# Performance work log

Hardware: AMD Instinct MI355X
Metric: run time of the kernel (lower is better)

## Reference

```python
import jax, jax.numpy as jnp
import numpy as np

B, H, W, C = 8, 64, 64, 64
C8 = C // 8

def setup_inputs() -> dict:
    key = jax.random.key(0)
    ks = jax.random.split(key, 5)
    x = jax.random.normal(ks[0], (B, H, W, C), dtype=jnp.float32)
    # 1x1 conv kernels (fan-in scaled) + biases
    wq = jax.random.normal(ks[1], (C, C8), dtype=jnp.float32) / np.sqrt(C)
    wk = jax.random.normal(ks[2], (C, C8), dtype=jnp.float32) / np.sqrt(C)
    wv = jax.random.normal(ks[3], (C, C), dtype=jnp.float32) / np.sqrt(C)
    bq = jnp.zeros((C8,), dtype=jnp.float32)
    bk = jnp.zeros((C8,), dtype=jnp.float32)
    bv = jnp.zeros((C,), dtype=jnp.float32)
    gamma = jax.random.normal(ks[4], (), dtype=jnp.float32)
    return {"x": x, "wq": wq, "bq": bq, "wk": wk, "bk": bk,
            "wv": wv, "bv": bv, "gamma": gamma}

def reference(x, wq, bq, wk, bk, wv, bv, gamma):
    b, h, w, c = x.shape
    n = h * w
    # 1x1 convs == per-pixel linear projections
    q = (jnp.einsum('bhwc,cd->bhwd', x, wq) + bq).reshape(b, n, -1)  # [B,N,C/8]
    k = (jnp.einsum('bhwc,cd->bhwd', x, wk) + bk).reshape(b, n, -1)  # [B,N,C/8]
    v = (jnp.einsum('bhwc,cd->bhwd', x, wv) + bv).reshape(b, n, -1)  # [B,N,C]
    # Unscaled attention: softmax over keys (last axis), no 1/sqrt(d)
    attn = jax.nn.softmax(jnp.einsum('bnd,bmd->bnm', q, k), axis=-1)  # [B,N,N]
    out = jnp.einsum('bnm,bmc->bnc', attn, v).reshape(b, h, w, c)
    return out * gamma + x
```

## Files before the change

### kernel.cpp

```cpp
#include <hip/hip_runtime.h>
#include <hip/hip_bf16.h>


#define BB 8
#define NN 4096
#define CC 64
#define PSTRIDE 72
#define LOG2E 1.44269504088896f

typedef _Float16 f16;
typedef _Float16 half8 __attribute__((ext_vector_type(8)));
typedef _Float16 half4 __attribute__((ext_vector_type(4)));
typedef __fp16 fp16x2 __attribute__((ext_vector_type(2)));
typedef float floatx4 __attribute__((ext_vector_type(4)));

static __device__ inline half4 pack4(float a, float b, float c, float d) {
    fp16x2 lo = __builtin_amdgcn_cvt_pkrtz(a, b);
    fp16x2 hi = __builtin_amdgcn_cvt_pkrtz(c, d);
    unsigned int lou = __builtin_bit_cast(unsigned int, lo);
    unsigned int hiu = __builtin_bit_cast(unsigned int, hi);
    unsigned long long packed = (unsigned long long)lou | ((unsigned long long)hiu << 32);
    return __builtin_bit_cast(half4, packed);
}


__global__ __launch_bounds__(256) void proj_all_kernel(
    const float* __restrict__ x,
    const float* __restrict__ wq, const float* __restrict__ bq,
    const float* __restrict__ wk, const float* __restrict__ bk,
    const float* __restrict__ wv, const float* __restrict__ bv,
    f16* __restrict__ Qh, f16* __restrict__ Kf, f16* __restrict__ Vf,
    float* __restrict__ qn2, float* __restrict__ kn2)
{
    __shared__ alignas(16) f16 Ws[80][PSTRIDE];
    __shared__ float Bs[80];
    __shared__ alignas(16) f16 Vs[64][68];
    __shared__ alignas(16) f16 Ks[64][12];
    const int tid = threadIdx.x;

    for (int i = tid; i < 4096; i += 256) {
        int cin = i >> 6, cout = i & 63;
        Ws[cout][cin] = (f16)wv[i];
    }
    for (int i = tid; i < 512; i += 256) {
        int cin = i >> 3, c = i & 7;
        Ws[64 + c][cin] = (f16)(wq[i] * LOG2E);
        Ws[72 + c][cin] = (f16)wk[i];
    }
    if (tid < 80)
        Bs[tid] = (tid < 64) ? bv[tid]
                : (tid < 72 ? bq[tid - 64] * LOG2E : bk[tid - 72]);
    __syncthreads();

    const int wave = tid >> 6, lane = tid & 63;
    const int quad = lane >> 4, n16 = lane & 15;
    const long pb = (long)blockIdx.x * 64;
    const long p0 = pb + wave * 16;
    const int  b   = (int)(pb >> 12);
    const int  nnb = (int)(pb & 4095);

    half8 ax[2];
#pragma unroll
    for (int kh = 0; kh < 2; ++kh) {
        const float* xp = x + (p0 + n16) * 64 + kh * 32 + quad * 8;
        float4 x1 = *(const float4*)xp;
        float4 x2 = *(const float4*)(xp + 4);
        ax[kh][0] = (f16)x1.x; ax[kh][1] = (f16)x1.y;
        ax[kh][2] = (f16)x1.z; ax[kh][3] = (f16)x1.w;
        ax[kh][4] = (f16)x2.x; ax[kh][5] = (f16)x2.y;
        ax[kh][6] = (f16)x2.z; ax[kh][7] = (f16)x2.w;
    }

#pragma unroll
    for (int ct = 0; ct < 5; ++ct) {
        const int cout = (ct < 4) ? ct * 16 + n16 : 64 + n16;
        const float bias = Bs[cout];
        half8 b0 = *(const half8*)(&Ws[cout][quad * 8]);
        half8 b1 = *(const half8*)(&Ws[cout][32 + quad * 8]);
        floatx4 acc = {bias, bias, bias, bias};
        acc = __builtin_amdgcn_mfma_f32_16x16x32_f16(ax[0], b0, acc, 0, 0, 0);
        acc = __builtin_amdgcn_mfma_f32_16x16x32_f16(ax[1], b1, acc, 0, 0, 0);
        if (ct < 4) {
#pragma unroll
            for (int r = 0; r < 4; ++r)
                Vs[wave * 16 + quad * 4 + r][ct * 16 + n16] = (f16)acc[r];
        } else {
            float n2[4];
#pragma unroll
            for (int r = 0; r < 4; ++r) n2[r] = acc[r] * acc[r];
#pragma unroll
            for (int d = 1; d < 8; d <<= 1)
#pragma unroll
                for (int r = 0; r < 4; ++r) n2[r] += __shfl_xor(n2[r], d, 64);
            if (n16 == 0) {
#pragma unroll
                for (int r = 0; r < 4; ++r) qn2[p0 + quad * 4 + r] = n2[r];
            } else if (n16 == 8) {
#pragma unroll
                for (int r = 0; r < 4; ++r) kn2[p0 + quad * 4 + r] = n2[r];
            }
            if (n16 < 8) {
                f16* dst = Qh + (p0 + quad * 4) * 8 + n16;
#pragma unroll
                for (int r = 0; r < 4; ++r) dst[r * 8] = (f16)acc[r];
            } else {
#pragma unroll
                for (int r = 0; r < 4; ++r)
                    Ks[wave * 16 + quad * 4 + r][n16 - 8] = (f16)acc[r];
            }
        }
    }
    __syncthreads();

#pragma unroll
    for (int u = 0; u < 2; ++u) {
        const int tt = wave * 2 + u;
        const int kb = tt >> 2, ct = tt & 3;
        half8 v;
#pragma unroll
        for (int j = 0; j < 4; ++j)
            v[j] = Vs[kb * 32 + quad * 4 + j][ct * 16 + n16];
#pragma unroll
        for (int j = 0; j < 4; ++j)
            v[4 + j] = Vs[kb * 32 + 16 + quad * 4 + j][ct * 16 + n16];
        const size_t kbg = (size_t)b * 128 + (nnb >> 5) + kb;
        *(half8*)(Vf + (kbg * 4 + ct) * 512 + lane * 8) = v;
    }
    if (wave < 2) {
        half8 kp;
#pragma unroll
        for (int e = 0; e < 2; ++e) {
            const int t = wave * 2 + e;
#pragma unroll
            for (int j = 0; j < 4; ++j) {
                f16 v = (f16)0.f;
                if (quad < 2) v = Ks[t * 16 + n16][quad * 4 + j];
                else if (quad == 2 && j == 0) v = (f16)1.f;
                kp[e * 4 + j] = v;
            }
        }
        const size_t kpg = (size_t)b * 128 + (nnb >> 5) + wave;
        *(half8*)(Kf + kpg * 512 + lane * 8) = kp;
    }
}

__global__ __launch_bounds__(256) void knorm_max_kernel(
    const float* __restrict__ kn2, float* __restrict__ Mk2)
{
    __shared__ float red[4];
    const int b = blockIdx.x, tid = threadIdx.x;
    float mx = 0.f;
    for (int i = tid; i < NN; i += 256) mx = fmaxf(mx, kn2[(size_t)b * NN + i]);
#pragma unroll
    for (int d = 1; d < 64; d <<= 1) mx = fmaxf(mx, __shfl_xor(mx, d, 64));
    if ((tid & 63) == 0) red[tid >> 6] = mx;
    __syncthreads();
    if (tid == 0) Mk2[b] = fmaxf(fmaxf(red[0], red[1]), fmaxf(red[2], red[3]));
}

__global__ __launch_bounds__(256, 3) void attn_kernel(
    const f16* __restrict__ Qh, const f16* __restrict__ Kf,
    const f16* __restrict__ Vf,
    const float* __restrict__ qn2, const float* __restrict__ Mk2,
    const float* __restrict__ x, const float* __restrict__ gptr,
    float* __restrict__ out)
{
    __shared__ alignas(16) char smem[30720];
    __shared__ float Ls[4][2][16];
    float* Obuf = (float*)smem;

    const int tid  = threadIdx.x;
    const int wave = tid >> 6, lane = tid & 63;
    const int quad = lane >> 4, n16 = lane & 15;
    const int ks = wave;

    const int b  = blockIdx.x & 7;
    const int qt = blockIdx.x >> 3;
    const size_t bN = (size_t)b * NN;

    const float mk2 = Mk2[b];

    half4 bq4[2];
#pragma unroll
    for (int qt2 = 0; qt2 < 2; ++qt2) {
        const int q = qt * 32 + qt2 * 16 + n16;
        const float mf = __builtin_sqrtf(qn2[bN + q] * mk2) - 12.0f;
        half4 v = {0, 0, 0, 0};
        if (quad < 2)
            v = *(const half4*)(Qh + (bN + q) * 8 + quad * 4);
        else if (quad == 2)
            v[0] = (f16)(-mf);
        bq4[qt2] = v;
    }

    floatx4 oacc[2][4];
#pragma unroll
    for (int qt2 = 0; qt2 < 2; ++qt2)
#pragma unroll
        for (int ct = 0; ct < 4; ++ct) oacc[qt2][ct] = (floatx4){0.f, 0.f, 0.f, 0.f};
    float l_loc[2] = {0.f, 0.f};

    const f16* kfb = Kf + ((size_t)b * 128 + ks * 32) * 512 + lane * 8;
    const f16* vfb = Vf + ((size_t)b * 128 + ks * 32) * 2048 + lane * 8;
    const floatx4 zero4 = {0.f, 0.f, 0.f, 0.f};

    half8 kkc0 = *(const half8*)(kfb + 0);
    half8 kkc1 = *(const half8*)(kfb + 512);

    for (int it = 0; it < 16; ++it) {
        half8 avp[2][4];
#pragma unroll
        for (int p = 0; p < 2; ++p)
#pragma unroll
            for (int ct = 0; ct < 4; ++ct)
                avp[p][ct] = *(const half8*)(vfb + ((size_t)(it * 2 + p) * 4 + ct) * 512);

        half4 ak[4];
        ak[0] = __builtin_shufflevector(kkc0, kkc0, 0, 1, 2, 3);
        ak[1] = __builtin_shufflevector(kkc0, kkc0, 4, 5, 6, 7);
        ak[2] = __builtin_shufflevector(kkc1, kkc1, 0, 1, 2, 3);
        ak[3] = __builtin_shufflevector(kkc1, kkc1, 4, 5, 6, 7);

        const int itn = (it < 15) ? it + 1 : 15;
        kkc0 = *(const half8*)(kfb + (size_t)itn * 1024);
        kkc1 = *(const half8*)(kfb + (size_t)itn * 1024 + 512);

#pragma unroll
        for (int qt2 = 0; qt2 < 2; ++qt2) {
            floatx4 sf[4];
#pragma unroll
            for (int t = 0; t < 4; ++t)
                sf[t] = __builtin_amdgcn_mfma_f32_16x16x16f16(ak[t], bq4[qt2], zero4, 0, 0, 0);

            half4 pk[4];
            float rst[4];
#pragma unroll
            for (int t = 0; t < 4; ++t) {
                float p0 = __builtin_exp2f(sf[t][0]);
                float p1 = __builtin_exp2f(sf[t][1]);
                float p2 = __builtin_exp2f(sf[t][2]);
                float p3 = __builtin_exp2f(sf[t][3]);
                rst[t] = (p0 + p1) + (p2 + p3);
                pk[t] = pack4(p0, p1, p2, p3);
            }
            l_loc[qt2] += (rst[0] + rst[1]) + (rst[2] + rst[3]);

#pragma unroll
            for (int t = 0; t < 4; ++t) {
                const int p = t >> 1;
#pragma unroll
                for (int ct = 0; ct < 4; ++ct) {
                    half4 va = (t & 1)
                        ? __builtin_shufflevector(avp[p][ct], avp[p][ct], 4, 5, 6, 7)
                        : __builtin_shufflevector(avp[p][ct], avp[p][ct], 0, 1, 2, 3);
                    oacc[qt2][ct] = __builtin_amdgcn_mfma_f32_16x16x16f16(va, pk[t], oacc[qt2][ct], 0, 0, 0);
                }
            }
        }
    }

    float l_run[2];
#pragma unroll
    for (int qt2 = 0; qt2 < 2; ++qt2) {
        float l = l_loc[qt2];
        l += __shfl_xor(l, 16, 64);
        l += __shfl_xor(l, 32, 64);
        l_run[qt2] = l;
    }

    __syncthreads();
    if (ks > 0) {
#pragma unroll
        for (int qt2 = 0; qt2 < 2; ++qt2) {
            if (quad == 0) Ls[ks][qt2][n16] = l_run[qt2];
            float* ob = Obuf + (size_t)(((ks - 1) * 2 + qt2) * 64 + lane) * 20;
#pragma unroll
            for (int ct = 0; ct < 4; ++ct)
                *(floatx4*)(ob + ct * 4) = oacc[qt2][ct];
        }
    }
    __syncthreads();
    if (ks == 0) {
        const float g = gptr[0];
#pragma unroll
        for (int qt2 = 0; qt2 < 2; ++qt2) {
            float l = l_run[qt2];
            float o[16];
#pragma unroll
            for (int ct = 0; ct < 4; ++ct)
#pragma unroll
                for (int r = 0; r < 4; ++r) o[ct * 4 + r] = oacc[qt2][ct][r];
#pragma unroll
            for (int p = 1; p < 4; ++p) {
                l += Ls[p][qt2][n16];
                const float* ob = Obuf + (size_t)(((p - 1) * 2 + qt2) * 64 + lane) * 20;
#pragma unroll
                for (int ct = 0; ct < 4; ++ct) {
                    floatx4 t = *(const floatx4*)(ob + ct * 4);
                    o[ct * 4 + 0] += t[0]; o[ct * 4 + 1] += t[1];
                    o[ct * 4 + 2] += t[2]; o[ct * 4 + 3] += t[3];
                }
            }
            const float scale = g / l;
            const int q = qt * 32 + qt2 * 16 + n16;
#pragma unroll
            for (int ct = 0; ct < 4; ++ct) {
                const size_t idx = (bN + q) * CC + ct * 16 + quad * 4;
                float4 xr = *(const float4*)(x + idx);
                float4 res;
                res.x = o[ct * 4 + 0] * scale + xr.x;
                res.y = o[ct * 4 + 1] * scale + xr.y;
                res.z = o[ct * 4 + 2] * scale + xr.z;
                res.w = o[ct * 4 + 3] * scale + xr.w;
                *(float4*)(out + idx) = res;
            }
        }
    }
}

extern "C" void kernel_launch(void* const* d_in, const int* in_sizes, int n_in,
                              void* d_out, int out_size, void* d_ws, size_t ws_size,
                              hipStream_t stream) {
    const float* x     = (const float*)d_in[0];
    const float* wq    = (const float*)d_in[1];
    const float* bq    = (const float*)d_in[2];
    const float* wk    = (const float*)d_in[3];
    const float* bk    = (const float*)d_in[4];
    const float* wv    = (const float*)d_in[5];
    const float* bv    = (const float*)d_in[6];
    const float* gamma = (const float*)d_in[7];
    float* out = (float*)d_out;

    f16* Qh = (f16*)d_ws;
    f16* Kf = Qh + (size_t)BB * NN * 8;
    f16* Vf = Kf + (size_t)BB * 128 * 512;
    float* qn2 = (float*)(Vf + (size_t)BB * 128 * 4 * 512);
    float* kn2 = qn2 + (size_t)BB * NN;
    float* Mk2 = kn2 + (size_t)BB * NN;

    proj_all_kernel<<<512, 256, 0, stream>>>(x, wq, bq, wk, bk, wv, bv,
                                             Qh, Kf, Vf, qn2, kn2);
    knorm_max_kernel<<<BB, 256, 0, stream>>>(kn2, Mk2);
    attn_kernel<<<BB * 128, 256, 0, stream>>>(Qh, Kf, Vf, qn2, Mk2, x, gamma, out);
}
```

Measured before the change: 123.9 us.

## Fuse key-norm max into projection kernel via atomicMax, vectorize LDS staging

Drops the separate knorm_max kernel. Each projection block now reduces its key squared norms and does an atomicMax on the per-batch max (as uint bits, valid because the values are non-negative), with a memset beforehand. The V staging buffer is transposed so LDS writes and reads use half4 vectors, and the weight loads use float4. This saves one kernel launch and the kn2 round trip through global memory, in exchange for a memset and atomic contention across 64 blocks per batch.

```diff
diff --git a/kernel.cpp b/kernel.cpp
--- a/kernel.cpp
+++ b/kernel.cpp
@@ -30,22 +30,37 @@
     const float* __restrict__ wk, const float* __restrict__ bk,
     const float* __restrict__ wv, const float* __restrict__ bv,
     f16* __restrict__ Qh, f16* __restrict__ Kf, f16* __restrict__ Vf,
-    float* __restrict__ qn2, float* __restrict__ kn2)
+    float* __restrict__ qn2, float* __restrict__ Mk2)
 {
     __shared__ alignas(16) f16 Ws[80][PSTRIDE];
     __shared__ float Bs[80];
-    __shared__ alignas(16) f16 Vs[64][68];
+    __shared__ alignas(16) f16 Vst[64][68];
     __shared__ alignas(16) f16 Ks[64][12];
+    __shared__ float redK[4];
     const int tid = threadIdx.x;
 
-    for (int i = tid; i < 4096; i += 256) {
-        int cin = i >> 6, cout = i & 63;
-        Ws[cout][cin] = (f16)wv[i];
-    }
-    for (int i = tid; i < 512; i += 256) {
-        int cin = i >> 3, c = i & 7;
-        Ws[64 + c][cin] = (f16)(wq[i] * LOG2E);
-        Ws[72 + c][cin] = (f16)wk[i];
+    for (int i4 = tid; i4 < 1024; i4 += 256) {
+        const int i = i4 * 4;
+        const int cin = i >> 6, cout = i & 63;
+        const float4 w = *(const float4*)(wv + i);
+        Ws[cout + 0][cin] = (f16)w.x;
+        Ws[cout + 1][cin] = (f16)w.y;
+        Ws[cout + 2][cin] = (f16)w.z;
+        Ws[cout + 3][cin] = (f16)w.w;
+    }
+    if (tid < 128) {
+        const int i = tid * 4;
+        const int cin = i >> 3, c = i & 7;
+        const float4 a = *(const float4*)(wq + i);
+        const float4 k = *(const float4*)(wk + i);
+        Ws[64 + c + 0][cin] = (f16)(a.x * LOG2E);
+        Ws[64 + c + 1][cin] = (f16)(a.y * LOG2E);
+        Ws[64 + c + 2][cin] = (f16)(a.z * LOG2E);
+        Ws[64 + c + 3][cin] = (f16)(a.w * LOG2E);
+        Ws[72 + c + 0][cin] = (f16)k.x;
+        Ws[72 + c + 1][cin] = (f16)k.y;
+        Ws[72 + c + 2][cin] = (f16)k.z;
+        Ws[72 + c + 3][cin] = (f16)k.w;
     }
     if (tid < 80)
         Bs[tid] = (tid < 64) ? bv[tid]
@@ -81,9 +96,8 @@
         acc = __builtin_amdgcn_mfma_f32_16x16x32_f16(ax[0], b0, acc, 0, 0, 0);
         acc = __builtin_amdgcn_mfma_f32_16x16x32_f16(ax[1], b1, acc, 0, 0, 0);
         if (ct < 4) {
-#pragma unroll
-            for (int r = 0; r < 4; ++r)
-                Vs[wave * 16 + quad * 4 + r][ct * 16 + n16] = (f16)acc[r];
+            half4 vp = {(f16)acc[0], (f16)acc[1], (f16)acc[2], (f16)acc[3]};
+            *(half4*)(&Vst[ct * 16 + n16][wave * 16 + quad * 4]) = vp;
         } else {
             float n2[4];
 #pragma unroll
@@ -95,10 +109,11 @@
             if (n16 == 0) {
 #pragma unroll
                 for (int r = 0; r < 4; ++r) qn2[p0 + quad * 4 + r] = n2[r];
-            } else if (n16 == 8) {
-#pragma unroll
-                for (int r = 0; r < 4; ++r) kn2[p0 + quad * 4 + r] = n2[r];
-            }
+            }
+            float km = fmaxf(fmaxf(n2[0], n2[1]), fmaxf(n2[2], n2[3]));
+            km = fmaxf(km, __shfl_xor(km, 16, 64));
+            km = fmaxf(km, __shfl_xor(km, 32, 64));
+            if (n16 == 8) redK[wave] = km;
             if (n16 < 8) {
                 f16* dst = Qh + (p0 + quad * 4) * 8 + n16;
 #pragma unroll
@@ -111,51 +126,38 @@
         }
     }
     __syncthreads();
+
+    if (tid == 0) {
+        float m = fmaxf(fmaxf(redK[0], redK[1]), fmaxf(redK[2], redK[3]));
+        atomicMax((unsigned int*)&Mk2[b], __float_as_uint(m));
+    }
 
 #pragma unroll
     for (int u = 0; u < 2; ++u) {
         const int tt = wave * 2 + u;
         const int kb = tt >> 2, ct = tt & 3;
-        half8 v;
-#pragma unroll
-        for (int j = 0; j < 4; ++j)
-            v[j] = Vs[kb * 32 + quad * 4 + j][ct * 16 + n16];
-#pragma unroll
-        for (int j = 0; j < 4; ++j)
-            v[4 + j] = Vs[kb * 32 + 16 + quad * 4 + j][ct * 16 + n16];
+        half4 lo = *(const half4*)(&Vst[ct * 16 + n16][kb * 32 + quad * 4]);
+        half4 hi = *(const half4*)(&Vst[ct * 16 + n16][kb * 32 + 16 + quad * 4]);
+        half8 v = {lo[0], lo[1], lo[2], lo[3], hi[0], hi[1], hi[2], hi[3]};
         const size_t kbg = (size_t)b * 128 + (nnb >> 5) + kb;
         *(half8*)(Vf + (kbg * 4 + ct) * 512 + lane * 8) = v;
     }
     if (wave < 2) {
-        half8 kp;
+        half8 kp = {0, 0, 0, 0, 0, 0, 0, 0};
 #pragma unroll
         for (int e = 0; e < 2; ++e) {
             const int t = wave * 2 + e;
-#pragma unroll
-            for (int j = 0; j < 4; ++j) {
-                f16 v = (f16)0.f;
-                if (quad < 2) v = Ks[t * 16 + n16][quad * 4 + j];
-                else if (quad == 2 && j == 0) v = (f16)1.f;
-                kp[e * 4 + j] = v;
+            if (quad < 2) {
+                half4 kd = *(const half4*)(&Ks[t * 16 + n16][quad * 4]);
+                kp[e * 4 + 0] = kd[0]; kp[e * 4 + 1] = kd[1];
+                kp[e * 4 + 2] = kd[2]; kp[e * 4 + 3] = kd[3];
+            } else if (quad == 2) {
+                kp[e * 4 + 0] = (f16)1.f;
             }
         }
         const size_t kpg = (size_t)b * 128 + (nnb >> 5) + wave;
         *(half8*)(Kf + kpg * 512 + lane * 8) = kp;
     }
-}
-
-__global__ __launch_bounds__(256) void knorm_max_kernel(
-    const float* __restrict__ kn2, float* __restrict__ Mk2)
-{
-    __shared__ float red[4];
-    const int b = blockIdx.x, tid = threadIdx.x;
-    float mx = 0.f;
-    for (int i = tid; i < NN; i += 256) mx = fmaxf(mx, kn2[(size_t)b * NN + i]);
-#pragma unroll
-    for (int d = 1; d < 64; d <<= 1) mx = fmaxf(mx, __shfl_xor(mx, d, 64));
-    if ((tid & 63) == 0) red[tid >> 6] = mx;
-    __syncthreads();
-    if (tid == 0) Mk2[b] = fmaxf(fmaxf(red[0], red[1]), fmaxf(red[2], red[3]));
 }
 
 __global__ __launch_bounds__(256, 3) void attn_kernel(
@@ -338,8 +340,8 @@
     float* kn2 = qn2 + (size_t)BB * NN;
     float* Mk2 = kn2 + (size_t)BB * NN;
 
+    hipMemsetAsync(Mk2, 0, BB * sizeof(float), stream);
     proj_all_kernel<<<512, 256, 0, stream>>>(x, wq, bq, wk, bk, wv, bv,
-                                             Qh, Kf, Vf, qn2, kn2);
-    knorm_max_kernel<<<BB, 256, 0, stream>>>(kn2, Mk2);
+                                             Qh, Kf, Vf, qn2, Mk2);
     attn_kernel<<<BB * 128, 256, 0, stream>>>(Qh, Kf, Vf, qn2, Mk2, x, gamma, out);
 }
```

New measurement: 125.9 us. Within noise of the previous version (+1.6%).
